# Performance work log

Measured on AMD Instinct MI355X. Metric: run time of the kernel, lower is better.

The kernel has to match this reference:

```python
import jax, jax.numpy as jnp
import numpy as np

QUERY_SHAPE = (128, 24)
MEM_FLANGE = (8, 8)
N_HEADS = 8
D_MODEL = 32


def _conv2d(x, w, b=None):
    # x: [B,H,W,Cin], w: [kh,kw,Cin,Cout], SAME padding, stride 1
    y = jax.lax.conv_general_dilated(x, w, window_strides=(1, 1), padding='SAME',
                                     dimension_numbers=('NHWC', 'HWIO', 'NHWC'))
    return y if b is None else y + b


def _local_attention_2d(q, k, v, query_shape, memory_flange):
    # q,k,v: [B, n_heads, H, W, d_head]; q is pre-scaled.
    B, n, H, W, d = q.shape
    qh, qw = query_shape
    fh, fw = memory_flange
    pad_h = (-H) % qh
    pad_w = (-W) % qw
    pad5 = ((0, 0), (0, 0), (0, pad_h), (0, pad_w), (0, 0))
    q = jnp.pad(q, pad5)
    k = jnp.pad(k, pad5)
    v = jnp.pad(v, pad5)
    Hq, Wq = H + pad_h, W + pad_w
    flange = ((0, 0), (0, 0), (fh, fh), (fw, fw), (0, 0))
    k = jnp.pad(k, flange)
    v = jnp.pad(v, flange)
    nH, nW = Hq // qh, Wq // qw
    mh, mw = qh + 2 * fh, qw + 2 * fw
    # Query blocks: [B, n, nH*nW, qh*qw, d]
    qb = q.reshape(B, n, nH, qh, nW, qw, d).transpose(0, 1, 2, 4, 3, 5, 6)
    qb = qb.reshape(B, n, nH * nW, qh * qw, d)
    # Overlapping memory blocks gathered from flange-padded k/v.
    rows = jnp.arange(nH)[:, None] * qh + jnp.arange(mh)[None, :]  # [nH, mh]
    cols = jnp.arange(nW)[:, None] * qw + jnp.arange(mw)[None, :]  # [nW, mw]
    kb = k[:, :, rows[:, None, :, None], cols[None, :, None, :], :]  # [B,n,nH,nW,mh,mw,d]
    vb = v[:, :, rows[:, None, :, None], cols[None, :, None, :], :]
    kb = kb.reshape(B, n, nH * nW, mh * mw, d)
    vb = vb.reshape(B, n, nH * nW, mh * mw, d)
    # t2t embedding_to_padding: mask positions whose key embedding is all-zero (the padding).
    bias = jnp.where(jnp.sum(jnp.abs(kb), axis=-1) == 0.0, -1e9, 0.0)[:, :, :, None, :]
    logits = jnp.einsum('bngqd,bngkd->bngqk', qb, kb) + bias
    attn = jax.nn.softmax(logits, axis=-1)
    ob = jnp.einsum('bngqk,bngkd->bngqd', attn, vb)
    out = ob.reshape(B, n, nH, nW, qh, qw, d).transpose(0, 1, 2, 4, 3, 5, 6)
    out = out.reshape(B, n, Hq, Wq, d)
    return out[:, :, :H, :W, :]


def _forward(x, wq, bq, wk, bk, wv, bv, wo):
    B, H, W, _ = x.shape
    dh = D_MODEL // N_HEADS

    def split_heads(t):  # [B,H,W,d_model] -> [B,n,H,W,dh]
        return t.reshape(B, H, W, N_HEADS, dh).transpose(0, 3, 1, 2, 4)

    q = split_heads(_conv2d(x, wq, bq)) * dh ** -0.5
    k = split_heads(_conv2d(x, wk, bk))
    v = split_heads(_conv2d(x, wv, bv))
    o = _local_attention_2d(q, k, v, QUERY_SHAPE, MEM_FLANGE)
    o = o.transpose(0, 2, 3, 1, 4).reshape(B, H, W, D_MODEL)  # combine heads
    return _conv2d(o, wo)  # no bias


def setup_inputs() -> dict:
    key = jax.random.key(0)
    ks = jax.random.split(key, 8)
    B, H, W, Cin, Cout = 1, 128, 48, 64, 64
    x = jax.random.normal(ks[0], (B, H, W, Cin), dtype=jnp.float32)

    def w(k, shape):
        fan_in = shape[0] * shape[1] * shape[2]
        return jax.random.normal(k, shape, dtype=jnp.float32) * (fan_in ** -0.5)

    return {
        'x': x,
        'wq': w(ks[1], (3, 3, Cin, D_MODEL)),
        'bq': jax.random.normal(ks[2], (D_MODEL,), dtype=jnp.float32) * 0.02,
        'wk': w(ks[3], (3, 3, Cin, D_MODEL)),
        'bk': jax.random.normal(ks[4], (D_MODEL,), dtype=jnp.float32) * 0.02,
        'wv': w(ks[5], (3, 3, Cin, D_MODEL)),
        'bv': jax.random.normal(ks[6], (D_MODEL,), dtype=jnp.float32) * 0.02,
        'wo': w(ks[7], (3, 3, D_MODEL, Cout)),
    }


def reference(x, wq, bq, wk, bk, wv, bv, wo):
    return _forward(x, wq, bq, wk, bk, wv, bv, wo)
```

## Files before the change

### kernel.cpp

```cpp
#include <hip/hip_runtime.h>

#define H_IMG 128
#define W_IMG 48
#define CIN   64
#define DM    32
#define NH    8
#define NPIX  6144
#define WPAD  50
#define HPAD  130

#define Q_SCALE 0.7213475204444817f

typedef _Float16 half4 __attribute__((ext_vector_type(4)));
typedef __fp16   fp16x2 __attribute__((ext_vector_type(2)));
typedef float    f32x4 __attribute__((ext_vector_type(4)));

__device__ __forceinline__ float fexp2(float x) { return __builtin_amdgcn_exp2f(x); }

__device__ __forceinline__ half4 exp_pack(f32x4 s) {
    fp16x2 lo = __builtin_amdgcn_cvt_pkrtz(fexp2(s[0]), fexp2(s[1]));
    fp16x2 hi = __builtin_amdgcn_cvt_pkrtz(fexp2(s[2]), fexp2(s[3]));
    half4 p;
    p[0] = (_Float16)lo[0]; p[1] = (_Float16)lo[1];
    p[2] = (_Float16)hi[0]; p[3] = (_Float16)hi[1];
    return p;
}

__global__ __launch_bounds__(256) void setup_kernel(
    const float* __restrict__ x,
    const float* __restrict__ wq, const float* __restrict__ wk,
    const float* __restrict__ wv, const float* __restrict__ wo,
    _Float16* __restrict__ xpad, _Float16* __restrict__ vT,
    _Float16* __restrict__ attpad,
    _Float16* __restrict__ whT, _Float16* __restrict__ whoT)
{
    const int bid = blockIdx.x;
    const int tid = threadIdx.x;

    if (bid < 26) {
        const int pp = bid * 256 + tid;
        if (pp < HPAD * WPAD) {
            const int py = pp / WPAD, px = pp % WPAD;
            _Float16* dst = xpad + (size_t)pp * CIN;
            if (py >= 1 && py <= H_IMG && px >= 1 && px <= W_IMG) {
                const float* src = x + ((size_t)(py - 1) * W_IMG + (px - 1)) * CIN;
                #pragma unroll
                for (int c = 0; c < CIN; c += 4) {
                    const float4 v = *reinterpret_cast<const float4*>(src + c);
                    half4 hv = { (_Float16)v.x, (_Float16)v.y, (_Float16)v.z, (_Float16)v.w };
                    *reinterpret_cast<half4*>(dst + c) = hv;
                }
            } else {
                const half4 z = {};
                #pragma unroll
                for (int c = 0; c < CIN; c += 4)
                    *reinterpret_cast<half4*>(dst + c) = z;
            }
        }
    } else if (bid == 26) {
        const int h = tid >> 5, chunk = tid & 31;
        _Float16* dst = vT + ((size_t)(h * 5 + 4)) * NPIX + chunk * (NPIX / 32);
        half4 ones = { (_Float16)1.0f, (_Float16)1.0f, (_Float16)1.0f, (_Float16)1.0f };
        #pragma unroll
        for (int i = 0; i < NPIX / 32; i += 4)
            *reinterpret_cast<half4*>(dst + i) = ones;
    } else if (bid < 53) {
        const int pp = (bid - 27) * 256 + tid;
        if (pp < HPAD * WPAD) {
            _Float16* dst = attpad + (size_t)pp * DM;
            const half4 z = {};
            #pragma unroll
            for (int c = 0; c < DM; c += 4)
                *reinterpret_cast<half4*>(dst + c) = z;
        }
    } else if (bid < 269) {
        const int u = (bid - 53) * 256 + tid;
        if (u < 3 * 32 * 576) {
            const int m    = u / 18432;
            const int rem  = u % 18432;
            const int c    = rem / 576;
            const int kidx = rem % 576;
            const int tap  = kidx / 64;
            const int ci   = kidx % 64;
            const float* w = (m == 0) ? wq : (m == 1) ? wk : wv;
            const float s  = (m == 0) ? Q_SCALE : 1.0f;
            whT[u] = (_Float16)(w[(size_t)tap * CIN * DM + (size_t)ci * DM + c] * s);
        }
    } else {
        const int u = (bid - 269) * 256 + tid;
        if (u < 64 * 288) {
            const int c    = u / 288;
            const int kidx = u % 288;
            const int tap  = kidx / 32;
            const int ci   = kidx % 32;
            whoT[u] = (_Float16)wo[(size_t)tap * DM * 64 + (size_t)ci * 64 + c];
        }
    }
}

__global__ __launch_bounds__(192) void qkv_mfma_kernel(
    const _Float16* __restrict__ xpad,
    const _Float16* __restrict__ whT,
    const float* __restrict__ bq, const float* __restrict__ bk,
    const float* __restrict__ bv,
    half4* __restrict__ qhi, half4* __restrict__ qlo,
    half4* __restrict__ khi, half4* __restrict__ klo,
    _Float16* __restrict__ vT)
{
    __shared__ f32x4 redq[2][64];
    __shared__ _Float16 lt[2][16][20];

    const int pt  = blockIdx.x % 384;
    const int ntm = blockIdx.x / 384;
    const int nt  = ntm % 2;
    const int m   = ntm / 2;
    const int wav = __builtin_amdgcn_readfirstlane(threadIdx.x >> 6);
    const int lane = threadIdx.x & 63;
    const int r    = lane & 15;
    const int g16  = lane >> 4;

    const int p  = pt * 16 + r;
    const int y  = p / W_IMG, x0 = p % W_IMG;
    const _Float16* xb = xpad + ((size_t)y * WPAD + x0) * CIN + 4 * g16;

    const int ch = nt * 16 + r;
    const _Float16* wb = whT + ((size_t)(m * 32 + ch)) * 576 + 4 * g16;

    f32x4 acc[4] = {{0.f,0.f,0.f,0.f},{0.f,0.f,0.f,0.f},
                    {0.f,0.f,0.f,0.f},{0.f,0.f,0.f,0.f}};

    const int dy = wav;
    #pragma unroll
    for (int dx = 0; dx < 3; ++dx) {
        const int toff = (dy * WPAD + dx) * CIN;
        const int k0   = (dy * 3 + dx) * 64;
        #pragma unroll
        for (int cb = 0; cb < 4; ++cb) {
            const half4 xa = *reinterpret_cast<const half4*>(xb + toff + cb * 16);
            const half4 wf = *reinterpret_cast<const half4*>(wb + k0 + cb * 16);
            acc[cb] = __builtin_amdgcn_mfma_f32_16x16x16f16(xa, wf, acc[cb], 0, 0, 0);
        }
    }

    f32x4 o = (acc[0] + acc[1]) + (acc[2] + acc[3]);

    if (wav > 0) redq[wav - 1][lane] = o;
    __syncthreads();
    if (wav != 0) return;

    o += redq[0][lane] + redq[1][lane];

    const float* b = (m == 0) ? bq : (m == 1) ? bk : bv;
    const float bias = b[ch] * ((m == 0) ? Q_SCALE : 1.0f);
    #pragma unroll
    for (int j = 0; j < 4; ++j) o[j] += bias;

    if (m == 2) {
        const int plane = (ch >> 2) * 5 + (ch & 3);
        const int pix0 = pt * 16 + 4 * g16;
        half4 hv = { (_Float16)o[0], (_Float16)o[1], (_Float16)o[2], (_Float16)o[3] };
        *reinterpret_cast<half4*>(vT + (size_t)plane * NPIX + pix0) = hv;
    } else {
        #pragma unroll
        for (int j = 0; j < 4; ++j) {
            const float val = o[j];
            const _Float16 hi = (_Float16)val;
            const _Float16 lo = (_Float16)(val - (float)hi);
            lt[0][4 * g16 + j][r] = hi;
            lt[1][4 * g16 + j][r] = lo;
        }
        const int p4 = lane & 15;
        const int hh = lane >> 4;
        const half4 hv = *reinterpret_cast<const half4*>(&lt[0][p4][hh * 4]);
        const half4 lv = *reinterpret_cast<const half4*>(&lt[1][p4][hh * 4]);
        const int h = nt * 4 + hh;
        const size_t idx = (size_t)h * NPIX + pt * 16 + p4;
        ((half4*)((m == 0) ? qhi : khi))[idx] = hv;
        ((half4*)((m == 0) ? qlo : klo))[idx] = lv;
    }
}

__global__ __launch_bounds__(1024) void attn_mfma_kernel(
    const half4* __restrict__ qhi, const half4* __restrict__ qlo,
    const half4* __restrict__ khi, const half4* __restrict__ klo,
    const _Float16* __restrict__ vT,
    _Float16* __restrict__ attpad)
{
    __shared__ f32x4 red[16][2][64];

    const int hg  = blockIdx.x / 48;
    const int qq  = blockIdx.x % 48;
    const int h   = hg >> 1, g = hg & 1;
    const int wav = __builtin_amdgcn_readfirstlane(threadIdx.x >> 6);
    const int seg = wav & 7;
    const int u   = wav >> 3;
    const int qt0 = qq * 4 + u * 2;
    const int lane = threadIdx.x & 63;
    const int c    = lane & 15;
    const int g16  = lane >> 4;
    const int c0   = g * 16;

    half4 qfA = {}, qfB = {};
    {
        const half4* qsrc = (g16 == 1) ? qlo : qhi;
        const int qa  = qt0 * 16 + c;
        const int qay = qa / 24;
        const int qb  = qa + 16;
        const int qby = qb / 24;
        if (g16 < 3) {
            qfA = qsrc[h * NPIX + qay * W_IMG + g * 24 + (qa - qay * 24)];
            qfB = qsrc[h * NPIX + qby * W_IMG + g * 24 + (qb - qby * 24)];
        }
    }

    const half4* kb = ((g16 == 2) ? klo : khi) + h * NPIX + c;
    const int vplane = (c < 4) ? c : 4;
    const _Float16* vb = vT + (h * 5 + vplane) * NPIX + 4 * g16;

    const f32x4 zc = {0.f, 0.f, 0.f, 0.f};
    f32x4 oA0 = zc, oA1 = zc, oB0 = zc, oB1 = zc;

    const int r0 = seg * 16;
    #pragma unroll 4
    for (int r = 0; r < 16; ++r) {
        const int koff = (r0 + r) * W_IMG + c0;

        const half4 k0 = kb[koff];
        const half4 k1 = kb[koff + 16];
        const half4 v0 = *reinterpret_cast<const half4*>(vb + koff);
        const half4 v1 = *reinterpret_cast<const half4*>(vb + koff + 16);

        const f32x4 sA0 = __builtin_amdgcn_mfma_f32_16x16x16f16(k0, qfA, zc, 0, 0, 0);
        const f32x4 sA1 = __builtin_amdgcn_mfma_f32_16x16x16f16(k1, qfA, zc, 0, 0, 0);
        const f32x4 sB0 = __builtin_amdgcn_mfma_f32_16x16x16f16(k0, qfB, zc, 0, 0, 0);
        const f32x4 sB1 = __builtin_amdgcn_mfma_f32_16x16x16f16(k1, qfB, zc, 0, 0, 0);

        const half4 pA0 = exp_pack(sA0);
        const half4 pA1 = exp_pack(sA1);
        const half4 pB0 = exp_pack(sB0);
        const half4 pB1 = exp_pack(sB1);

        oA0 = __builtin_amdgcn_mfma_f32_16x16x16f16(pA0, v0, oA0, 0, 0, 0);
        oA1 = __builtin_amdgcn_mfma_f32_16x16x16f16(pA1, v1, oA1, 0, 0, 0);
        oB0 = __builtin_amdgcn_mfma_f32_16x16x16f16(pB0, v0, oB0, 0, 0, 0);
        oB1 = __builtin_amdgcn_mfma_f32_16x16x16f16(pB1, v1, oB1, 0, 0, 0);
    }

    red[wav][0][lane] = oA0 + oA1;
    red[wav][1][lane] = oB0 + oB1;
    __syncthreads();

    if (wav < 4) {
        const int u2  = wav >> 1;
        const int t01 = wav & 1;
        f32x4 o = red[u2 * 8 + 0][t01][lane];
        #pragma unroll
        for (int s = 1; s < 8; ++s)
            o += red[u2 * 8 + s][t01][lane];

        const int baddr = (g16 * 16 + 4) << 2;
        f32x4 on;
        #pragma unroll
        for (int r = 0; r < 4; ++r) {
            const float ss = __int_as_float(
                __builtin_amdgcn_ds_bpermute(baddr, __float_as_int(o[r])));
            on[r] = o[r] * __builtin_amdgcn_rcpf(ss);
        }

        if (c < 4) {
            const int qt = qq * 4 + u2 * 2 + t01;
            #pragma unroll
            for (int r = 0; r < 4; ++r) {
                const int q  = qt * 16 + 4 * g16 + r;
                const int qy = q / 24;
                const int qx = g * 24 + (q - qy * 24);
                attpad[((size_t)(qy + 1) * WPAD + qx + 1) * DM + h * 4 + c] =
                    (_Float16)on[r];
            }
        }
    }
}

__global__ __launch_bounds__(192) void out_mfma_kernel(
    const _Float16* __restrict__ attpad,
    const _Float16* __restrict__ whoT,
    float* __restrict__ out)
{
    __shared__ f32x4 redo[2][64];

    const int pt  = blockIdx.x % 384;
    const int nt  = blockIdx.x / 384;
    const int wav = __builtin_amdgcn_readfirstlane(threadIdx.x >> 6);
    const int lane = threadIdx.x & 63;
    const int r    = lane & 15;
    const int g16  = lane >> 4;

    const int p  = pt * 16 + r;
    const int y  = p / W_IMG, x0 = p % W_IMG;
    const _Float16* ab = attpad + ((size_t)y * WPAD + x0) * DM + 4 * g16;

    const int ch = nt * 16 + r;
    const _Float16* wb = whoT + (size_t)ch * 288 + 4 * g16;

    f32x4 a0 = {0.f, 0.f, 0.f, 0.f}, a1 = {0.f, 0.f, 0.f, 0.f};

    const int dy = wav;
    #pragma unroll
    for (int dx = 0; dx < 3; ++dx) {
        const int toff = (dy * WPAD + dx) * DM;
        const int k0   = (dy * 3 + dx) * 32;
        const half4 xa0 = *reinterpret_cast<const half4*>(ab + toff);
        const half4 wf0 = *reinterpret_cast<const half4*>(wb + k0);
        a0 = __builtin_amdgcn_mfma_f32_16x16x16f16(xa0, wf0, a0, 0, 0, 0);
        const half4 xa1 = *reinterpret_cast<const half4*>(ab + toff + 16);
        const half4 wf1 = *reinterpret_cast<const half4*>(wb + k0 + 16);
        a1 = __builtin_amdgcn_mfma_f32_16x16x16f16(xa1, wf1, a1, 0, 0, 0);
    }

    f32x4 o = a0 + a1;
    if (wav > 0) redo[wav - 1][lane] = o;
    __syncthreads();
    if (wav != 0) return;

    o += redo[0][lane] + redo[1][lane];

    const int pix0 = pt * 16 + 4 * g16;
    #pragma unroll
    for (int j = 0; j < 4; ++j)
        out[(size_t)(pix0 + j) * 64 + nt * 16 + r] = o[j];
}

extern "C" void kernel_launch(void* const* d_in, const int* in_sizes, int n_in,
                              void* d_out, int out_size, void* d_ws, size_t ws_size,
                              hipStream_t stream)
{
    const float* x  = (const float*)d_in[0];
    const float* wq = (const float*)d_in[1];
    const float* bq = (const float*)d_in[2];
    const float* wk = (const float*)d_in[3];
    const float* bk = (const float*)d_in[4];
    const float* wv = (const float*)d_in[5];
    const float* bv = (const float*)d_in[6];
    const float* wo = (const float*)d_in[7];
    float* out = (float*)d_out;

    char* base = (char*)d_ws;
    half4*    qhi    = (half4*)(base + 0);
    half4*    qlo    = (half4*)(base + 393216);
    half4*    khi    = (half4*)(base + 786432);
    half4*    klo    = (half4*)(base + 1179648);
    _Float16* vT     = (_Float16*)(base + 1572864);
    _Float16* xpad   = (_Float16*)(base + 2064384);
    _Float16* attpad = (_Float16*)(base + 2896384);
    _Float16* whT    = (_Float16*)(base + 3312384);
    _Float16* whoT   = (_Float16*)(base + 3422976);

    hipLaunchKernelGGL(setup_kernel, dim3(341), dim3(256), 0, stream,
                       x, wq, wk, wv, wo, xpad, vT, attpad, whT, whoT);

    hipLaunchKernelGGL(qkv_mfma_kernel, dim3(2304), dim3(192), 0, stream,
                       xpad, whT, bq, bk, bv, qhi, qlo, khi, klo, vT);

    hipLaunchKernelGGL(attn_mfma_kernel, dim3(16 * 48), dim3(1024), 0, stream,
                       qhi, qlo, khi, klo, vT, attpad);

    hipLaunchKernelGGL(out_mfma_kernel, dim3(4 * 384), dim3(192), 0, stream,
                       attpad, whoT, out);
}
```

Before: 68.80 us.

## Remove setup kernel by fusing fp16 conversion and padding into compute kernels

Drops the separate setup launch that built a padded fp16 copy of x, transposed fp16 weights, the ones plane for V and the zeroed attention border. The QKV conv now reads fp32 x with bounds checks and converts weights on the fly. The ones plane is written by idle waves in the QKV kernel, and the attpad border is zeroed inside the attention kernel. This saves a launch and an extra round trip through memory, but adds strided scalar weight loads and per-element conversions inside the MFMA loops.

Measured after the change: 56.54 us. 1.22x faster.

```diff
diff --git a/kernel.cpp b/kernel.cpp
--- a/kernel.cpp
+++ b/kernel.cpp
@@ -26,83 +26,11 @@
     return p;
 }
 
-__global__ __launch_bounds__(256) void setup_kernel(
+__global__ __launch_bounds__(192) void qkv_mfma_kernel(
     const float* __restrict__ x,
-    const float* __restrict__ wq, const float* __restrict__ wk,
-    const float* __restrict__ wv, const float* __restrict__ wo,
-    _Float16* __restrict__ xpad, _Float16* __restrict__ vT,
-    _Float16* __restrict__ attpad,
-    _Float16* __restrict__ whT, _Float16* __restrict__ whoT)
-{
-    const int bid = blockIdx.x;
-    const int tid = threadIdx.x;
-
-    if (bid < 26) {
-        const int pp = bid * 256 + tid;
-        if (pp < HPAD * WPAD) {
-            const int py = pp / WPAD, px = pp % WPAD;
-            _Float16* dst = xpad + (size_t)pp * CIN;
-            if (py >= 1 && py <= H_IMG && px >= 1 && px <= W_IMG) {
-                const float* src = x + ((size_t)(py - 1) * W_IMG + (px - 1)) * CIN;
-                #pragma unroll
-                for (int c = 0; c < CIN; c += 4) {
-                    const float4 v = *reinterpret_cast<const float4*>(src + c);
-                    half4 hv = { (_Float16)v.x, (_Float16)v.y, (_Float16)v.z, (_Float16)v.w };
-                    *reinterpret_cast<half4*>(dst + c) = hv;
-                }
-            } else {
-                const half4 z = {};
-                #pragma unroll
-                for (int c = 0; c < CIN; c += 4)
-                    *reinterpret_cast<half4*>(dst + c) = z;
-            }
-        }
-    } else if (bid == 26) {
-        const int h = tid >> 5, chunk = tid & 31;
-        _Float16* dst = vT + ((size_t)(h * 5 + 4)) * NPIX + chunk * (NPIX / 32);
-        half4 ones = { (_Float16)1.0f, (_Float16)1.0f, (_Float16)1.0f, (_Float16)1.0f };
-        #pragma unroll
-        for (int i = 0; i < NPIX / 32; i += 4)
-            *reinterpret_cast<half4*>(dst + i) = ones;
-    } else if (bid < 53) {
-        const int pp = (bid - 27) * 256 + tid;
-        if (pp < HPAD * WPAD) {
-            _Float16* dst = attpad + (size_t)pp * DM;
-            const half4 z = {};
-            #pragma unroll
-            for (int c = 0; c < DM; c += 4)
-                *reinterpret_cast<half4*>(dst + c) = z;
-        }
-    } else if (bid < 269) {
-        const int u = (bid - 53) * 256 + tid;
-        if (u < 3 * 32 * 576) {
-            const int m    = u / 18432;
-            const int rem  = u % 18432;
-            const int c    = rem / 576;
-            const int kidx = rem % 576;
-            const int tap  = kidx / 64;
-            const int ci   = kidx % 64;
-            const float* w = (m == 0) ? wq : (m == 1) ? wk : wv;
-            const float s  = (m == 0) ? Q_SCALE : 1.0f;
-            whT[u] = (_Float16)(w[(size_t)tap * CIN * DM + (size_t)ci * DM + c] * s);
-        }
-    } else {
-        const int u = (bid - 269) * 256 + tid;
-        if (u < 64 * 288) {
-            const int c    = u / 288;
-            const int kidx = u % 288;
-            const int tap  = kidx / 32;
-            const int ci   = kidx % 32;
-            whoT[u] = (_Float16)wo[(size_t)tap * DM * 64 + (size_t)ci * 64 + c];
-        }
-    }
-}
-
-__global__ __launch_bounds__(192) void qkv_mfma_kernel(
-    const _Float16* __restrict__ xpad,
-    const _Float16* __restrict__ whT,
-    const float* __restrict__ bq, const float* __restrict__ bk,
-    const float* __restrict__ bv,
+    const float* __restrict__ wq, const float* __restrict__ bq,
+    const float* __restrict__ wk, const float* __restrict__ bk,
+    const float* __restrict__ wv, const float* __restrict__ bv,
     half4* __restrict__ qhi, half4* __restrict__ qlo,
     half4* __restrict__ khi, half4* __restrict__ klo,
     _Float16* __restrict__ vT)
@@ -119,25 +47,34 @@
     const int r    = lane & 15;
     const int g16  = lane >> 4;
 
-    const int p  = pt * 16 + r;
-    const int y  = p / W_IMG, x0 = p % W_IMG;
-    const _Float16* xb = xpad + ((size_t)y * WPAD + x0) * CIN + 4 * g16;
+    const int y   = pt / 3;
+    const int x0c = (pt % 3) * 16 + r;
+    const int yy  = y + wav - 1;
+    const bool vrow = (yy >= 0) && (yy < H_IMG);
 
     const int ch = nt * 16 + r;
-    const _Float16* wb = whT + ((size_t)(m * 32 + ch)) * 576 + 4 * g16;
+    const float* w = (m == 0) ? wq : (m == 1) ? wk : wv;
+    const float  s = (m == 0) ? Q_SCALE : 1.0f;
 
     f32x4 acc[4] = {{0.f,0.f,0.f,0.f},{0.f,0.f,0.f,0.f},
                     {0.f,0.f,0.f,0.f},{0.f,0.f,0.f,0.f}};
 
-    const int dy = wav;
     #pragma unroll
     for (int dx = 0; dx < 3; ++dx) {
-        const int toff = (dy * WPAD + dx) * CIN;
-        const int k0   = (dy * 3 + dx) * 64;
+        const int xx = x0c + dx - 1;
+        const bool v = vrow && (xx >= 0) && (xx < W_IMG);
+        const int poff = v ? (yy * W_IMG + xx) : 0;
+        const float* xsrc = x + (size_t)poff * CIN + 4 * g16;
+        const float* wp0  = w + (size_t)(wav * 3 + dx) * CIN * DM + 4 * g16 * DM + ch;
         #pragma unroll
         for (int cb = 0; cb < 4; ++cb) {
-            const half4 xa = *reinterpret_cast<const half4*>(xb + toff + cb * 16);
-            const half4 wf = *reinterpret_cast<const half4*>(wb + k0 + cb * 16);
+            f32x4 xv = {0.f, 0.f, 0.f, 0.f};
+            if (v) xv = *reinterpret_cast<const f32x4*>(xsrc + cb * 16);
+            half4 xa = { (_Float16)xv[0], (_Float16)xv[1],
+                         (_Float16)xv[2], (_Float16)xv[3] };
+            const float* wp = wp0 + cb * 16 * DM;
+            half4 wf = { (_Float16)(wp[0 * DM] * s), (_Float16)(wp[1 * DM] * s),
+                         (_Float16)(wp[2 * DM] * s), (_Float16)(wp[3 * DM] * s) };
             acc[cb] = __builtin_amdgcn_mfma_f32_16x16x16f16(xa, wf, acc[cb], 0, 0, 0);
         }
     }
@@ -146,12 +83,19 @@
 
     if (wav > 0) redq[wav - 1][lane] = o;
     __syncthreads();
-    if (wav != 0) return;
+    if (wav != 0) {
+        if (wav == 1 && m == 2) {
+            const int pix = pt * 16 + (lane & 15);
+            const int h   = nt * 4 + (lane >> 4);
+            vT[(size_t)(h * 5 + 4) * NPIX + pix] = (_Float16)1.0f;
+        }
+        return;
+    }
 
     o += redq[0][lane] + redq[1][lane];
 
     const float* b = (m == 0) ? bq : (m == 1) ? bk : bv;
-    const float bias = b[ch] * ((m == 0) ? Q_SCALE : 1.0f);
+    const float bias = b[ch] * s;
     #pragma unroll
     for (int j = 0; j < 4; ++j) o[j] += bias;
 
@@ -200,6 +144,20 @@
     const int g16  = lane >> 4;
     const int c0   = g * 16;
 
+    if (hg == 0 && wav == 0) {
+        const int i = qq * 8 + (lane >> 3);
+        if (i < 356) {
+            int py, px;
+            if (i < 50)       { py = 0;              px = i; }
+            else if (i < 100) { py = HPAD - 1;       px = i - 50; }
+            else if (i < 228) { py = 1 + (i - 100);  px = 0; }
+            else              { py = 1 + (i - 228);  px = WPAD - 1; }
+            const half4 z = {};
+            *reinterpret_cast<half4*>(
+                attpad + ((size_t)py * WPAD + px) * DM + (lane & 7) * 4) = z;
+        }
+    }
+
     half4 qfA = {}, qfB = {};
     {
         const half4* qsrc = (g16 == 1) ? qlo : qhi;
@@ -283,7 +241,7 @@
 
 __global__ __launch_bounds__(192) void out_mfma_kernel(
     const _Float16* __restrict__ attpad,
-    const _Float16* __restrict__ whoT,
+    const float* __restrict__ wo,
     float* __restrict__ out)
 {
     __shared__ f32x4 redo[2][64];
@@ -295,26 +253,29 @@
     const int r    = lane & 15;
     const int g16  = lane >> 4;
 
-    const int p  = pt * 16 + r;
-    const int y  = p / W_IMG, x0 = p % W_IMG;
+    const int y   = pt / 3;
+    const int x0  = (pt % 3) * 16 + r;
     const _Float16* ab = attpad + ((size_t)y * WPAD + x0) * DM + 4 * g16;
 
     const int ch = nt * 16 + r;
-    const _Float16* wb = whoT + (size_t)ch * 288 + 4 * g16;
 
     f32x4 a0 = {0.f, 0.f, 0.f, 0.f}, a1 = {0.f, 0.f, 0.f, 0.f};
 
-    const int dy = wav;
     #pragma unroll
     for (int dx = 0; dx < 3; ++dx) {
-        const int toff = (dy * WPAD + dx) * DM;
-        const int k0   = (dy * 3 + dx) * 32;
-        const half4 xa0 = *reinterpret_cast<const half4*>(ab + toff);
-        const half4 wf0 = *reinterpret_cast<const half4*>(wb + k0);
-        a0 = __builtin_amdgcn_mfma_f32_16x16x16f16(xa0, wf0, a0, 0, 0, 0);
-        const half4 xa1 = *reinterpret_cast<const half4*>(ab + toff + 16);
-        const half4 wf1 = *reinterpret_cast<const half4*>(wb + k0 + 16);
-        a1 = __builtin_amdgcn_mfma_f32_16x16x16f16(xa1, wf1, a1, 0, 0, 0);
+        const int toff = (wav * WPAD + dx) * DM;
+        const float* wp0 = wo + (size_t)(wav * 3 + dx) * DM * 64 + 4 * g16 * 64 + ch;
+        #pragma unroll
+        for (int cb = 0; cb < 2; ++cb) {
+            const half4 xa = *reinterpret_cast<const half4*>(ab + toff + cb * 16);
+            const float* wp = wp0 + cb * 16 * 64;
+            half4 wf = { (_Float16)wp[0 * 64], (_Float16)wp[1 * 64],
+                         (_Float16)wp[2 * 64], (_Float16)wp[3 * 64] };
+            if (cb & 1)
+                a1 = __builtin_amdgcn_mfma_f32_16x16x16f16(xa, wf, a1, 0, 0, 0);
+            else
+                a0 = __builtin_amdgcn_mfma_f32_16x16x16f16(xa, wf, a0, 0, 0, 0);
+        }
     }
 
     f32x4 o = a0 + a1;
@@ -350,20 +311,14 @@
     half4*    khi    = (half4*)(base + 786432);
     half4*    klo    = (half4*)(base + 1179648);
     _Float16* vT     = (_Float16*)(base + 1572864);
-    _Float16* xpad   = (_Float16*)(base + 2064384);
-    _Float16* attpad = (_Float16*)(base + 2896384);
-    _Float16* whT    = (_Float16*)(base + 3312384);
-    _Float16* whoT   = (_Float16*)(base + 3422976);
-
-    hipLaunchKernelGGL(setup_kernel, dim3(341), dim3(256), 0, stream,
-                       x, wq, wk, wv, wo, xpad, vT, attpad, whT, whoT);
+    _Float16* attpad = (_Float16*)(base + 2064384);
 
     hipLaunchKernelGGL(qkv_mfma_kernel, dim3(2304), dim3(192), 0, stream,
-                       xpad, whT, bq, bk, bv, qhi, qlo, khi, klo, vT);
+                       x, wq, bq, wk, bk, wv, bv, qhi, qlo, khi, klo, vT);
 
     hipLaunchKernelGGL(attn_mfma_kernel, dim3(16 * 48), dim3(1024), 0, stream,
                        qhi, qlo, khi, klo, vT, attpad);
 
     hipLaunchKernelGGL(out_mfma_kernel, dim3(4 * 384), dim3(192), 0, stream,
-                       attpad, whoT, out);
-}
+                       attpad, wo, out);
+}
```
